# Kernel tuning notes

Measured on AMD Instinct MI355X. Metric: run time of the kernel, lower is better.

Reference implementation:

```python
import jax, jax.numpy as jnp
import numpy as np

NEG_INF = -1e9  # additive mask value for masked softmax


def setup_inputs() -> dict:
    key = jax.random.key(0)
    k1, k2, k3, k4, k5 = jax.random.split(key, 5)
    bz, rv_num, rv_len, in_feat, out_feat = 32, 10, 128, 300, 128
    seq_a = jax.random.normal(k1, (bz, rv_num, rv_len, in_feat), dtype=jnp.float32)
    seq_b = jax.random.normal(k2, (bz, rv_num, rv_len, in_feat), dtype=jnp.float32)
    mask_a = jax.random.randint(k3, (bz, rv_num, rv_len), 0, 2, dtype=jnp.int32)
    mask_b = jax.random.randint(k4, (bz, rv_num, rv_len), 0, 2, dtype=jnp.int32)
    # guarantee at least one valid position per review (avoid fully-masked rows)
    mask_a = mask_a.at[:, :, 0].set(1)
    mask_b = mask_b.at[:, :, 0].set(1)
    # FC transform params (xavier-normal-ish weight, zero bias)
    W = jax.random.normal(k5, (in_feat, out_feat), dtype=jnp.float32) * (2.0 / np.sqrt(in_feat + out_feat))
    b = jnp.zeros((out_feat,), dtype=jnp.float32)
    return {"seq_a": seq_a, "seq_b": seq_b, "mask_a": mask_a, "mask_b": mask_b, "W": W, "b": b}


def _masked_softmax(scores, mask):
    # scores: [N, L], mask: [N, L] in {0,1}
    logits = jnp.where(mask > 0, scores, NEG_INF)
    return jax.nn.softmax(logits, axis=-1)


def reference(seq_a, seq_b, mask_a, mask_b, W, b):
    bz, rv_num, rv_len, _ = seq_a.shape
    hdim = W.shape[1]
    N = bz * rv_num          # flattened batch of reviews
    M = rv_num * rv_len      # all tokens on the other side

    # FC + ReLU feature transform
    ta = jax.nn.relu(jnp.einsum('bnld,dh->bnlh', seq_a, W) + b)
    tb = jax.nn.relu(jnp.einsum('bnld,dh->bnlh', seq_b, W) + b)

    sa = ta.reshape(N, rv_len, hdim)
    sb = tb.reshape(N, rv_len, hdim)
    # expand: each review attends over ALL tokens of the other sequence in its sample
    ea = jnp.broadcast_to(ta.reshape(bz, 1, M, hdim), (bz, rv_num, M, hdim)).reshape(N, M, hdim)
    eb = jnp.broadcast_to(tb.reshape(bz, 1, M, hdim), (bz, rv_num, M, hdim)).reshape(N, M, hdim)

    # DOT interaction (no scale): affinity [N, rv_len, M]
    atob_aff = jnp.einsum('nld,nmd->nlm', sa, eb)
    btoa_aff = jnp.einsum('nld,nmd->nlm', sb, ea)

    # MEAN pooling over the other-sequence axis
    atob_scores = atob_aff.mean(axis=-1)  # [N, rv_len]
    btoa_scores = btoa_aff.mean(axis=-1)

    ma = mask_a.reshape(N, rv_len)
    mb = mask_b.reshape(N, rv_len)
    atob_w = _masked_softmax(atob_scores, ma)
    btoa_w = _masked_softmax(btoa_scores, mb)

    a_out = jnp.einsum('nl,nld->nd', atob_w, sa)
    b_out = jnp.einsum('nl,nld->nd', btoa_w, sb)
    return (a_out, b_out, atob_w, btoa_w)
```

## Files before the change

kernel.cpp:

```cpp
#include <hip/hip_runtime.h>
#include <hip/hip_bf16.h>


#define K_FEAT 300
#define H 128
#define NTOK 40960
#define NREV 320
#define TOK_PER_SAMPLE 1280
#define TM 32
#define FC_BLKS_PER_SIDE 1280
#define FC_BLKS_PER_SAMPLE 40
#define NCHUNK 10
#define WFRAG_ELEMS (NCHUNK * 4 * 2 * 64 * 8)

typedef _Float16 f16;
typedef __attribute__((ext_vector_type(8))) _Float16 f16x8;
typedef __attribute__((ext_vector_type(4))) float f32x4;
typedef unsigned short u16;
typedef unsigned int u32;

static __device__ __forceinline__ u16 f2bf(float x) {
    u32 u = __float_as_uint(x);
    return (u16)((u + 0x7fffu + ((u >> 16) & 1u)) >> 16);
}
static __device__ __forceinline__ float bf2f(u16 s) {
    return __uint_as_float(((u32)s) << 16);
}
static __device__ __forceinline__ u16 f2h_bits(float x) {
    f16 h = (f16)x;
    return *(u16*)&h;
}
static __device__ __forceinline__ u32 pk2h(float a, float b) {
    return (u32)f2h_bits(a) | ((u32)f2h_bits(b) << 16);
}

__global__ void wsplit_kernel(const float* __restrict__ W, u16* __restrict__ Wfrag)
{
    int i = blockIdx.x * 256 + threadIdx.x;
    if (i >= WFRAG_ELEMS) return;
    int j    = i & 7;
    int lane = (i >> 3) & 63;
    int t2   = (i >> 9) & 1;
    int p    = (i >> 10) & 3;
    int c    = i >> 12;
    int nn = lane & 15, quad = lane >> 4;
    int h = (2 * p + t2) * 16 + nn;
    int k = c * 32 + quad * 8 + j;
    float w = (k < K_FEAT) ? W[(size_t)k * H + h] : 0.f;
    Wfrag[i] = f2h_bits(w);
}

__global__ __launch_bounds__(256, 4) void fc_mfma_kernel(
    const float* __restrict__ seq_a, const float* __restrict__ seq_b,
    const u16* __restrict__ Wfrag, const float* __restrict__ bias,
    u16* __restrict__ ta, u16* __restrict__ tb,
    float* __restrict__ psum_a, float* __restrict__ psum_b)
{
    int blk = blockIdx.x;
    const float* seq; u16* outp; float* psum;
    if (blk < FC_BLKS_PER_SIDE) { seq = seq_a; outp = ta; psum = psum_a; }
    else { seq = seq_b; outp = tb; psum = psum_b; blk -= FC_BLKS_PER_SIDE; }

    const int tid = threadIdx.x;
    const int tok0 = blk * TM;
    const int wave = tid >> 6;
    const int lane = tid & 63;
    const int nn = lane & 15;
    const int quad = lane >> 4;

    const float* rowA0 = seq + (size_t)(tok0 + nn) * K_FEAT + quad * 8;
    const float* rowA1 = rowA0 + (size_t)16 * K_FEAT;
    const u16* wbase = Wfrag + (size_t)wave * 1024 + (size_t)lane * 8;

    f32x4 acc[2][2];
#pragma unroll
    for (int m = 0; m < 2; ++m) {
        acc[m][0] = (f32x4){0.f, 0.f, 0.f, 0.f};
        acc[m][1] = (f32x4){0.f, 0.f, 0.f, 0.f};
    }

#pragma unroll
    for (int c = 0; c < NCHUNK; ++c) {
        f16x8 wh0 = *(const f16x8*)&wbase[(size_t)c * 4096];
        f16x8 wh1 = *(const f16x8*)&wbase[(size_t)c * 4096 + 512];
#pragma unroll
        for (int m = 0; m < 2; ++m) {
            const float* r = (m == 0) ? rowA0 : rowA1;
            float4 af0, af1;
            if (c < 9) {
                af0 = *(const float4*)(r + c * 32);
                af1 = *(const float4*)(r + c * 32 + 4);
            } else {
                af0 = make_float4(0.f, 0.f, 0.f, 0.f);
                af1 = make_float4(0.f, 0.f, 0.f, 0.f);
                if (quad < 2)  af0 = *(const float4*)(r + c * 32);
                if (quad == 0) af1 = *(const float4*)(r + c * 32 + 4);
            }
            uint4 pkt;
            pkt.x = pk2h(af0.x, af0.y);
            pkt.y = pk2h(af0.z, af0.w);
            pkt.z = pk2h(af1.x, af1.y);
            pkt.w = pk2h(af1.z, af1.w);
            f16x8 a = *reinterpret_cast<f16x8*>(&pkt);
            acc[m][0] = __builtin_amdgcn_mfma_f32_16x16x32_f16(wh0, a, acc[m][0], 0, 0, 0);
            acc[m][1] = __builtin_amdgcn_mfma_f32_16x16x32_f16(wh1, a, acc[m][1], 0, 0, 0);
        }
    }

#pragma unroll
    for (int ht = 0; ht < 2; ++ht) {
        const int h0 = (2 * wave + ht) * 16 + quad * 4;
        const float4 bb = *(const float4*)&bias[h0];
        float fs[4] = {0.f, 0.f, 0.f, 0.f};
#pragma unroll
        for (int m = 0; m < 2; ++m) {
            int tok = tok0 + m * 16 + nn;
            float v0 = fmaxf(acc[m][ht][0] + bb.x, 0.f);
            float v1 = fmaxf(acc[m][ht][1] + bb.y, 0.f);
            float v2 = fmaxf(acc[m][ht][2] + bb.z, 0.f);
            float v3 = fmaxf(acc[m][ht][3] + bb.w, 0.f);
            fs[0] += v0; fs[1] += v1; fs[2] += v2; fs[3] += v3;
            uint2 pk;
            pk.x = (u32)f2bf(v0) | ((u32)f2bf(v1) << 16);
            pk.y = (u32)f2bf(v2) | ((u32)f2bf(v3) << 16);
            *(uint2*)&outp[(size_t)tok * H + h0] = pk;
        }
#pragma unroll
        for (int r = 0; r < 4; ++r) {
            fs[r] += __shfl_xor(fs[r], 1);
            fs[r] += __shfl_xor(fs[r], 2);
            fs[r] += __shfl_xor(fs[r], 4);
            fs[r] += __shfl_xor(fs[r], 8);
        }
        if (nn == 0) {
#pragma unroll
            for (int r = 0; r < 4; ++r)
                psum[(size_t)blk * H + h0 + r] = fs[r];
        }
    }
}

__global__ __launch_bounds__(512) void attn_kernel(
    const u16* __restrict__ ta, const u16* __restrict__ tb,
    const int* __restrict__ mask_a, const int* __restrict__ mask_b,
    const float* __restrict__ psum_a, const float* __restrict__ psum_b,
    float* __restrict__ out)
{
    int n = blockIdx.x;
    int side = 0;
    if (n >= NREV) { side = 1; n -= NREV; }

    const u16* t = side ? tb : ta;
    const int* mask = side ? mask_b : mask_a;
    const float* psum_o = side ? psum_a : psum_b;
    float* out_vec = out + (side ? NREV * H : 0);
    float* out_w = out + 2 * NREV * H + (side ? NREV * H : 0);

    int sample = n / 10;
    int tid = threadIdx.x;

    __shared__ __align__(16) u16 T_s[128 * 128];
    __shared__ float fbuf[32 * 128];
    __shared__ float mean_s[128];
    __shared__ float w_s[128];
    __shared__ float red[8];

    if (tid < 128) {
        const float* pb = psum_o + (size_t)sample * FC_BLKS_PER_SAMPLE * H + tid;
        float s0 = 0.f, s1 = 0.f, s2 = 0.f, s3 = 0.f;
#pragma unroll
        for (int i = 0; i < FC_BLKS_PER_SAMPLE; i += 4) {
            s0 += pb[(size_t)(i + 0) * H];
            s1 += pb[(size_t)(i + 1) * H];
            s2 += pb[(size_t)(i + 2) * H];
            s3 += pb[(size_t)(i + 3) * H];
        }
        mean_s[tid] = (s0 + s1 + s2 + s3) * (1.0f / (float)TOK_PER_SAMPLE);
    }
    __syncthreads();

    const u16* rowbase = t + (size_t)n * 128 * H;

#pragma unroll
    for (int i = 0; i < 4; ++i) {
        int q = tid + 512 * i;
        int r = q >> 4;
        int c8 = q & 15;
        uint4 v = *(const uint4*)&rowbase[r * H + c8 * 8];
        *(uint4*)&T_s[r * H + c8 * 8] = v;
        const float* m = &mean_s[c8 * 8];
        float p = 0.f;
        p += bf2f((u16)(v.x & 0xffff)) * m[0];
        p += bf2f((u16)(v.x >> 16)) * m[1];
        p += bf2f((u16)(v.y & 0xffff)) * m[2];
        p += bf2f((u16)(v.y >> 16)) * m[3];
        p += bf2f((u16)(v.z & 0xffff)) * m[4];
        p += bf2f((u16)(v.z >> 16)) * m[5];
        p += bf2f((u16)(v.w & 0xffff)) * m[6];
        p += bf2f((u16)(v.w >> 16)) * m[7];
        fbuf[r * 17 + c8] = p;
    }
    __syncthreads();

    float logit = -1e9f;
    if (tid < 128) {
        float s = 0.f;
#pragma unroll
        for (int j = 0; j < 16; ++j) s += fbuf[tid * 17 + j];
        int mv = mask[n * 128 + tid];
        logit = (mv > 0) ? s : -1e9f;
    }

    float mx = logit;
    for (int off = 32; off > 0; off >>= 1) mx = fmaxf(mx, __shfl_xor(mx, off));
    if ((tid & 63) == 0) red[tid >> 6] = mx;
    __syncthreads();
    mx = red[0];
#pragma unroll
    for (int rr = 1; rr < 8; ++rr) mx = fmaxf(mx, red[rr]);
    __syncthreads();

    float e = __expf(logit - mx);
    float ssum = e;
    for (int off = 32; off > 0; off >>= 1) ssum += __shfl_xor(ssum, off);
    if ((tid & 63) == 0) red[tid >> 6] = ssum;
    __syncthreads();
    ssum = 0.f;
#pragma unroll
    for (int rr = 0; rr < 8; ++rr) ssum += red[rr];

    float w = e / ssum;
    if (tid < 128) {
        w_s[tid] = w;
        out_w[n * 128 + tid] = w;
    }
    __syncthreads();

    int c8 = tid & 15;
    int lp = tid >> 4;
    float o[8] = {0.f, 0.f, 0.f, 0.f, 0.f, 0.f, 0.f, 0.f};
#pragma unroll
    for (int k = 0; k < 4; ++k) {
        int l = k * 32 + lp;
        float wl = w_s[l];
        uint4 v = *(const uint4*)&T_s[l * H + c8 * 8];
        o[0] = fmaf(wl, bf2f((u16)(v.x & 0xffff)), o[0]);
        o[1] = fmaf(wl, bf2f((u16)(v.x >> 16)), o[1]);
        o[2] = fmaf(wl, bf2f((u16)(v.y & 0xffff)), o[2]);
        o[3] = fmaf(wl, bf2f((u16)(v.y >> 16)), o[3]);
        o[4] = fmaf(wl, bf2f((u16)(v.z & 0xffff)), o[4]);
        o[5] = fmaf(wl, bf2f((u16)(v.z >> 16)), o[5]);
        o[6] = fmaf(wl, bf2f((u16)(v.w & 0xffff)), o[6]);
        o[7] = fmaf(wl, bf2f((u16)(v.w >> 16)), o[7]);
    }
    *(float4*)&fbuf[lp * 128 + c8 * 8] = make_float4(o[0], o[1], o[2], o[3]);
    *(float4*)&fbuf[lp * 128 + c8 * 8 + 4] = make_float4(o[4], o[5], o[6], o[7]);
    __syncthreads();
    if (tid < 128) {
        float s = 0.f;
#pragma unroll
        for (int p = 0; p < 32; ++p) s += fbuf[p * 128 + tid];
        out_vec[n * 128 + tid] = s;
    }
}

extern "C" void kernel_launch(void* const* d_in, const int* in_sizes, int n_in,
                              void* d_out, int out_size, void* d_ws, size_t ws_size,
                              hipStream_t stream)
{
    const float* seq_a = (const float*)d_in[0];
    const float* seq_b = (const float*)d_in[1];
    const int* mask_a = (const int*)d_in[2];
    const int* mask_b = (const int*)d_in[3];
    const float* W = (const float*)d_in[4];
    const float* bias = (const float*)d_in[5];
    float* out = (float*)d_out;

    u16* ta = (u16*)d_ws;
    u16* tb = ta + (size_t)NTOK * H;
    float* psum_a = (float*)(tb + (size_t)NTOK * H);
    float* psum_b = psum_a + FC_BLKS_PER_SIDE * H;
    u16* Wfrag = (u16*)(psum_b + FC_BLKS_PER_SIDE * H);

    wsplit_kernel<<<(WFRAG_ELEMS + 255) / 256, 256, 0, stream>>>(W, Wfrag);
    fc_mfma_kernel<<<2 * FC_BLKS_PER_SIDE, 256, 0, stream>>>(seq_a, seq_b, Wfrag, bias, ta, tb, psum_a, psum_b);
    attn_kernel<<<640, 512, 0, stream>>>(ta, tb, mask_a, mask_b, psum_a, psum_b, out);
}
```

Baseline: 175.0 us.

## Stage FC input tiles into LDS via async global_load_lds with XOR swizzle

The FC kernel now copies each 32-token input tile into shared memory with direct global-to-LDS loads. Each thread issues one 16-byte load per chunk, and rows are XOR-swizzled to avoid bank conflicts. The MFMA loop then reads A fragments from LDS instead of doing strided per-lane global loads. The last K chunk is shifted to start at column 268 so it stays in bounds, and the weight fragments are remapped to zero the overlapping columns. The aim is more coalesced global traffic, at the cost of 40KB of LDS per block, which may limit occupancy against the 4-blocks launch bound.

```diff
diff --git a/kernel.cpp b/kernel.cpp
--- a/kernel.cpp
+++ b/kernel.cpp
@@ -45,8 +45,14 @@
     int c    = i >> 12;
     int nn = lane & 15, quad = lane >> 4;
     int h = (2 * p + t2) * 16 + nn;
-    int k = c * 32 + quad * 8 + j;
-    float w = (k < K_FEAT) ? W[(size_t)k * H + h] : 0.f;
+    float w;
+    if (c < 9) {
+        int k = c * 32 + quad * 8 + j;
+        w = W[(size_t)k * H + h];
+    } else {
+        int k = 268 + quad * 8 + j;
+        w = (k >= 288) ? W[(size_t)k * H + h] : 0.f;
+    }
     Wfrag[i] = f2h_bits(w);
 }
 
@@ -56,6 +62,8 @@
     u16* __restrict__ ta, u16* __restrict__ tb,
     float* __restrict__ psum_a, float* __restrict__ psum_b)
 {
+    __shared__ __align__(16) float A_s[NCHUNK * 1024];
+
     int blk = blockIdx.x;
     const float* seq; u16* outp; float* psum;
     if (blk < FC_BLKS_PER_SIDE) { seq = seq_a; outp = ta; psum = psum_a; }
@@ -68,9 +76,22 @@
     const int nn = lane & 15;
     const int quad = lane >> 4;
 
-    const float* rowA0 = seq + (size_t)(tok0 + nn) * K_FEAT + quad * 8;
-    const float* rowA1 = rowA0 + (size_t)16 * K_FEAT;
-    const u16* wbase = Wfrag + (size_t)wave * 1024 + (size_t)lane * 8;
+    {
+        const int tok_s = tid >> 3;
+        const int s_raw = tid & 7;
+        const int s_log = s_raw ^ (tok_s & 7);
+        const float* gbase = seq + (size_t)(tok0 + tok_s) * K_FEAT + s_log * 4;
+#pragma unroll
+        for (int c = 0; c < NCHUNK; ++c) {
+            const float* gp = gbase + ((c < 9) ? c * 32 : 268);
+            float* lp = &A_s[c * 1024 + wave * 256];
+            __builtin_amdgcn_global_load_lds(
+                (const __attribute__((address_space(1))) u32*)gp,
+                (__attribute__((address_space(3))) u32*)lp,
+                16, 0, 0);
+        }
+    }
+    __syncthreads();
 
     f32x4 acc[2][2];
 #pragma unroll
@@ -79,28 +100,23 @@
         acc[m][1] = (f32x4){0.f, 0.f, 0.f, 0.f};
     }
 
+    const u16* wbase = Wfrag + (size_t)wave * 1024 + (size_t)lane * 8;
+    const int nn7 = nn & 7;
+
 #pragma unroll
     for (int c = 0; c < NCHUNK; ++c) {
         f16x8 wh0 = *(const f16x8*)&wbase[(size_t)c * 4096];
         f16x8 wh1 = *(const f16x8*)&wbase[(size_t)c * 4096 + 512];
 #pragma unroll
         for (int m = 0; m < 2; ++m) {
-            const float* r = (m == 0) ? rowA0 : rowA1;
-            float4 af0, af1;
-            if (c < 9) {
-                af0 = *(const float4*)(r + c * 32);
-                af1 = *(const float4*)(r + c * 32 + 4);
-            } else {
-                af0 = make_float4(0.f, 0.f, 0.f, 0.f);
-                af1 = make_float4(0.f, 0.f, 0.f, 0.f);
-                if (quad < 2)  af0 = *(const float4*)(r + c * 32);
-                if (quad == 0) af1 = *(const float4*)(r + c * 32 + 4);
-            }
+            const int rowf = c * 1024 + m * 512 + nn * 32;
+            float4 f0 = *(const float4*)&A_s[rowf + (((2 * quad)     ^ nn7) << 2)];
+            float4 f1 = *(const float4*)&A_s[rowf + (((2 * quad + 1) ^ nn7) << 2)];
             uint4 pkt;
-            pkt.x = pk2h(af0.x, af0.y);
-            pkt.y = pk2h(af0.z, af0.w);
-            pkt.z = pk2h(af1.x, af1.y);
-            pkt.w = pk2h(af1.z, af1.w);
+            pkt.x = pk2h(f0.x, f0.y);
+            pkt.y = pk2h(f0.z, f0.w);
+            pkt.z = pk2h(f1.x, f1.y);
+            pkt.w = pk2h(f1.z, f1.w);
             f16x8 a = *reinterpret_cast<f16x8*>(&pkt);
             acc[m][0] = __builtin_amdgcn_mfma_f32_16x16x32_f16(wh0, a, acc[m][0], 0, 0, 0);
             acc[m][1] = __builtin_amdgcn_mfma_f32_16x16x32_f16(wh1, a, acc[m][1], 0, 0, 0);
```

Measured after the change: 146.8 us. -16.1%, faster.
